# Performance work log

Measured on AMD Instinct MI355X. Metric: run time of the kernel, lower is better.

The kernel has to match this reference:

```python
import jax, jax.numpy as jnp
import numpy as np

N_NODES = 100000
N_EDGES = 3200000
IN_DIM = 128
OUT_DIM = 128


def setup_inputs() -> dict:
    key = jax.random.key(0)
    k1, k2, k3, k4, k5 = jax.random.split(key, 5)
    fea_input = jax.random.normal(k1, (N_NODES, IN_DIM), dtype=jnp.float32)
    edge_row = jax.random.randint(k2, (N_EDGES,), 0, N_NODES, dtype=jnp.int32)
    edge_col = jax.random.randint(k3, (N_EDGES,), 0, N_NODES, dtype=jnp.int32)
    edge_val = jax.random.uniform(k4, (N_EDGES,), dtype=jnp.float32)
    # kaiming_uniform-style init for weight, zeros for bias
    bound = float(np.sqrt(6.0 / IN_DIM))
    weight = jax.random.uniform(k5, (IN_DIM, OUT_DIM), dtype=jnp.float32,
                                minval=-bound, maxval=bound)
    bias = jnp.zeros((OUT_DIM,), dtype=jnp.float32)
    return {
        "fea_input": fea_input,
        "edge_row": edge_row,
        "edge_col": edge_col,
        "edge_val": edge_val,
        "weight": weight,
        "bias": bias,
    }


def reference(fea_input, edge_row, edge_col, edge_val, weight, bias):
    # support = X @ W  -> [N, OUT_DIM]
    support = jnp.matmul(fea_input, weight)
    # SpMM: out[r] += val * support[c] for each edge (r, c, val)
    gathered = support[edge_col] * edge_val[:, None]  # [E, OUT_DIM]
    output = jax.ops.segment_sum(gathered, edge_row, num_segments=N_NODES)
    return output + bias
```

## Files before the change

kernel.cpp:

```cpp
#include <hip/hip_runtime.h>
#include <hip/hip_bf16.h>


#define N_NODES 100000
#define N_EDGES 3200000
#define DIM 128
#define RB 16
#define RPB 128
#define NBKT ((N_NODES + RPB - 1) / RPB)
#define CHUNK 8192
#define NCHK ((N_EDGES + CHUNK - 1) / CHUNK)
#define CAP2 5376

typedef __attribute__((ext_vector_type(8))) short bf16x8;
typedef __attribute__((ext_vector_type(4))) float f32x4;
typedef unsigned long long u64;
typedef unsigned int u32;

__device__ inline ushort bf16rne(float f) {
  uint32_t u = __float_as_uint(f);
  u += 0x7fffu + ((u >> 16) & 1u);
  return (ushort)(u >> 16);
}
__device__ inline float lofl(u32 u) { return __uint_as_float(u << 16); }
__device__ inline float hifl(u32 u) { return __uint_as_float(u & 0xffff0000u); }

__global__ __launch_bounds__(256) void prep_count_kernel(
    const float* __restrict__ X, const float* __restrict__ W,
    ushort* __restrict__ Xh, ushort* __restrict__ Wh,
    const int* __restrict__ erow, int* __restrict__ bcnt,
    int* __restrict__ table) {
  __shared__ int cnt[NBKT];
  if (blockIdx.x < 1024) {
    const size_t nx4 = (size_t)N_NODES * DIM / 4;
    const size_t nw4 = (size_t)DIM * DIM / 4;
    for (size_t i = (size_t)blockIdx.x * blockDim.x + threadIdx.x;
         i < nx4 + nw4; i += (size_t)1024 * blockDim.x) {
      const float4 f = (i < nx4) ? ((const float4*)X)[i] : ((const float4*)W)[i - nx4];
      ushort4 h;
      h.x = bf16rne(f.x); h.y = bf16rne(f.y); h.z = bf16rne(f.z); h.w = bf16rne(f.w);
      if (i < nx4) ((ushort4*)Xh)[i] = h;
      else         ((ushort4*)Wh)[i - nx4] = h;
    }
  } else {
    const int cb = blockIdx.x - 1024;
    for (int b = threadIdx.x; b < NBKT; b += 256) cnt[b] = 0;
    __syncthreads();
    const int e0 = cb * CHUNK;
    #pragma unroll
    for (int it = 0; it < CHUNK / 256; ++it) {
      const int e = e0 + it * 256 + threadIdx.x;
      if (e < N_EDGES) atomicAdd(&cnt[erow[e] >> 7], 1);
    }
    __syncthreads();
    for (int b = threadIdx.x; b < NBKT; b += 256) {
      const int c = cnt[b];
      table[(size_t)cb * NBKT + b] = c;
      if (c) atomicAdd(&bcnt[b], c);
    }
  }
}

__global__ __launch_bounds__(1024) void bscan_kernel(int* __restrict__ bcur,
                                                     int* __restrict__ bbase) {
  __shared__ int wsum[16];
  const int t = threadIdx.x, lane = t & 63, wid = t >> 6;
  const int v = (t < NBKT) ? bcur[t] : 0;
  int incl = v;
  #pragma unroll
  for (int off = 1; off < 64; off <<= 1) {
    int n = __shfl_up(incl, off, 64);
    if (lane >= off) incl += n;
  }
  if (lane == 63) wsum[wid] = incl;
  __syncthreads();
  if (t == 0) {
    int s = 0;
    #pragma unroll
    for (int w = 0; w < 16; ++w) { int x = wsum[w]; wsum[w] = s; s += x; }
  }
  __syncthreads();
  const int excl = wsum[wid] + incl - v;
  if (t < NBKT) { bbase[t] = excl; bcur[t] = excl; }
  if (t == NBKT - 1) bbase[NBKT] = excl + v;
}

__global__ __launch_bounds__(256) void partition_kernel(
    const int* __restrict__ erow, const int* __restrict__ ecol,
    const float* __restrict__ eval, const int* __restrict__ table,
    int* __restrict__ bcur, u64* __restrict__ p64) {
  __shared__ int cnt[NBKT];
  const int e0 = blockIdx.x * CHUNK;
  for (int b = threadIdx.x; b < NBKT; b += 256) {
    const int c = table[(size_t)blockIdx.x * NBKT + b];
    cnt[b] = c ? atomicAdd(&bcur[b], c) : 0;
  }
  __syncthreads();
  #pragma unroll
  for (int it = 0; it < CHUNK / 256; ++it) {
    const int e = e0 + it * 256 + threadIdx.x;
    if (e < N_EDGES) {
      const int r = erow[e];
      const u32 lo = ((u32)ecol[e] << 15) | (u32)bf16rne(eval[e]);
      const int p = atomicAdd(&cnt[r >> 7], 1);
      p64[p] = ((u64)(r & (RPB - 1)) << 32) | (u64)lo;
    }
  }
}

__global__ __launch_bounds__(512) void agg_sort_kernel(
    const ushort* __restrict__ Xh,
    const int* __restrict__ bbase, const u64* __restrict__ p64,
    ushort* __restrict__ Yh) {
  __shared__ u32 sbuf[CAP2 + 16];
  __shared__ int hist[RPB];
  __shared__ int rstart[RPB];
  __shared__ int curs[RPB];
  __shared__ int wtot;
  const int b = blockIdx.x, t = threadIdx.x;
  const int s = bbase[b];
  int nE = bbase[b + 1] - s;
  if (nE > CAP2) nE = CAP2;

  if (t < RPB) hist[t] = 0;
  __syncthreads();
  for (int i = t; i < nE; i += 512)
    atomicAdd(&hist[(int)(p64[s + i] >> 32) & (RPB - 1)], 1);
  __syncthreads();
  int v = 0, incl = 0;
  if (t < RPB) {
    v = hist[t];
    incl = v;
    #pragma unroll
    for (int off = 1; off < 64; off <<= 1) {
      int n = __shfl_up(incl, off, 64);
      if ((t & 63) >= off) incl += n;
    }
    if (t == 63) wtot = incl;
  }
  __syncthreads();
  if (t < RPB) {
    const int e = incl - v + ((t >= 64) ? wtot : 0);
    rstart[t] = e;
    curs[t] = e;
  }
  __syncthreads();
  for (int i = t; i < nE; i += 512) {
    const u64 w = p64[s + i];
    const int p = atomicAdd(&curs[(int)(w >> 32) & (RPB - 1)], 1);
    sbuf[p] = (u32)w;
  }
  __syncthreads();

  const int wid = t >> 6, lane = t & 63;
  const int q = lane >> 4;
  const u32 sub16 = (u32)(lane & 15) * 16u;
  const char* Xb = (const char*)Xh;
  #pragma unroll 1
  for (int j = 0; j < 16; ++j) {
    const int rl = wid * 16 + j;
    const int gr = b * RPB + rl;
    if (gr >= N_NODES) break;
    const int s0 = rstart[rl];
    const int s1 = s0 + hist[rl];
    float f0 = 0.f, f1 = 0.f, f2 = 0.f, f3 = 0.f;
    float f4 = 0.f, f5 = 0.f, f6 = 0.f, f7 = 0.f;
    #pragma unroll 1
    for (int e = s0 + q; e < s1; e += 16) {
      const u32 lo0 = sbuf[e];
      const u32 lo1 = (e + 4  < s1) ? sbuf[e + 4]  : 0u;
      const u32 lo2 = (e + 8  < s1) ? sbuf[e + 8]  : 0u;
      const u32 lo3 = (e + 12 < s1) ? sbuf[e + 12] : 0u;
      const u32 o0 = (lo0 >> 7) & 0xFFFFFF00u;
      const u32 o1 = (lo1 >> 7) & 0xFFFFFF00u;
      const u32 o2 = (lo2 >> 7) & 0xFFFFFF00u;
      const u32 o3 = (lo3 >> 7) & 0xFFFFFF00u;
      const uint4 g0 = *(const uint4*)(Xb + (o0 + sub16));
      const uint4 g1 = *(const uint4*)(Xb + (o1 + sub16));
      const uint4 g2 = *(const uint4*)(Xb + (o2 + sub16));
      const uint4 g3 = *(const uint4*)(Xb + (o3 + sub16));
      const float v0 = __uint_as_float((lo0 & 0x7fffu) << 16);
      const float v1 = __uint_as_float((lo1 & 0x7fffu) << 16);
      const float v2 = __uint_as_float((lo2 & 0x7fffu) << 16);
      const float v3 = __uint_as_float((lo3 & 0x7fffu) << 16);
      f0 += v0 * lofl(g0.x); f1 += v0 * hifl(g0.x);
      f2 += v0 * lofl(g0.y); f3 += v0 * hifl(g0.y);
      f4 += v0 * lofl(g0.z); f5 += v0 * hifl(g0.z);
      f6 += v0 * lofl(g0.w); f7 += v0 * hifl(g0.w);
      f0 += v1 * lofl(g1.x); f1 += v1 * hifl(g1.x);
      f2 += v1 * lofl(g1.y); f3 += v1 * hifl(g1.y);
      f4 += v1 * lofl(g1.z); f5 += v1 * hifl(g1.z);
      f6 += v1 * lofl(g1.w); f7 += v1 * hifl(g1.w);
      f0 += v2 * lofl(g2.x); f1 += v2 * hifl(g2.x);
      f2 += v2 * lofl(g2.y); f3 += v2 * hifl(g2.y);
      f4 += v2 * lofl(g2.z); f5 += v2 * hifl(g2.z);
      f6 += v2 * lofl(g2.w); f7 += v2 * hifl(g2.w);
      f0 += v3 * lofl(g3.x); f1 += v3 * hifl(g3.x);
      f2 += v3 * lofl(g3.y); f3 += v3 * hifl(g3.y);
      f4 += v3 * lofl(g3.z); f5 += v3 * hifl(g3.z);
      f6 += v3 * lofl(g3.w); f7 += v3 * hifl(g3.w);
    }
    f0 += __shfl_xor(f0, 16); f1 += __shfl_xor(f1, 16);
    f2 += __shfl_xor(f2, 16); f3 += __shfl_xor(f3, 16);
    f4 += __shfl_xor(f4, 16); f5 += __shfl_xor(f5, 16);
    f6 += __shfl_xor(f6, 16); f7 += __shfl_xor(f7, 16);
    f0 += __shfl_xor(f0, 32); f1 += __shfl_xor(f1, 32);
    f2 += __shfl_xor(f2, 32); f3 += __shfl_xor(f3, 32);
    f4 += __shfl_xor(f4, 32); f5 += __shfl_xor(f5, 32);
    f6 += __shfl_xor(f6, 32); f7 += __shfl_xor(f7, 32);
    if (lane < 16) {
      uint4 o;
      o.x = (u32)bf16rne(f0) | ((u32)bf16rne(f1) << 16);
      o.y = (u32)bf16rne(f2) | ((u32)bf16rne(f3) << 16);
      o.z = (u32)bf16rne(f4) | ((u32)bf16rne(f5) << 16);
      o.w = (u32)bf16rne(f6) | ((u32)bf16rne(f7) << 16);
      ((uint4*)(Yh + (size_t)gr * DIM))[lane] = o;
    }
  }
}

__global__ __launch_bounds__(256) void gemm_mfma(const ushort* __restrict__ Yh,
                                                 const ushort* __restrict__ Wh,
                                                 const float* __restrict__ bias,
                                                 float* __restrict__ out) {
  const int wid = threadIdx.x >> 6, lane = threadIdx.x & 63;
  const int lr = lane & 15, lq = lane >> 4;
  const int n0 = wid * 32;

  bf16x8 bfrag[4][2];
  float bval[2];
  #pragma unroll
  for (int nt = 0; nt < 2; ++nt) {
    const int col = n0 + nt * 16 + lr;
    bval[nt] = bias[col];
    #pragma unroll
    for (int kk = 0; kk < 4; ++kk) {
      const int kbase = kk * 32 + lq * 8;
      bf16x8 b;
      #pragma unroll
      for (int i = 0; i < 8; ++i)
        b[i] = (short)Wh[(size_t)(kbase + i) * DIM + col];
      bfrag[kk][nt] = b;
    }
  }

  const int r0 = blockIdx.x * 256;
  #pragma unroll 1
  for (int g = 0; g < 16; ++g) {
    const int m0 = r0 + g * 16;
    if (m0 >= N_NODES) break;
    bf16x8 afrag[4];
    const ushort* arow = Yh + (size_t)(m0 + lr) * DIM + lq * 8;
    #pragma unroll
    for (int kk = 0; kk < 4; ++kk)
      afrag[kk] = *(const bf16x8*)(arow + kk * 32);
    #pragma unroll
    for (int nt = 0; nt < 2; ++nt) {
      f32x4 acc = {0.f, 0.f, 0.f, 0.f};
      #pragma unroll
      for (int kk = 0; kk < 4; ++kk)
        acc = __builtin_amdgcn_mfma_f32_16x16x32_bf16(afrag[kk], bfrag[kk][nt], acc, 0, 0, 0);
      const int col = n0 + nt * 16 + lr;
      #pragma unroll
      for (int j = 0; j < 4; ++j)
        out[(size_t)(m0 + lq * 4 + j) * DIM + col] = acc[j] + bval[nt];
    }
  }
}

__global__ __launch_bounds__(128) void gemm_kernel(
    const float* __restrict__ IN, const float* __restrict__ W,
    float* __restrict__ OUT, const float* __restrict__ bias, int add_bias) {
  __shared__ float Wsh[DIM * DIM];
  __shared__ float Xsh[RB * DIM];
  const int t = threadIdx.x;
  #pragma unroll 8
  for (int i = 0; i < DIM; ++i) Wsh[i * DIM + t] = W[i * DIM + t];
  const int r0 = blockIdx.x * RB;
  #pragma unroll
  for (int idx = t; idx < RB * DIM; idx += 128)
    Xsh[idx] = IN[(size_t)r0 * DIM + idx];
  __syncthreads();
  float acc[RB];
  const float b = add_bias ? bias[t] : 0.f;
  #pragma unroll
  for (int r = 0; r < RB; ++r) acc[r] = b;
  for (int k = 0; k < DIM; ++k) {
    const float w = Wsh[k * DIM + t];
    #pragma unroll
    for (int r = 0; r < RB; ++r) acc[r] += Xsh[r * DIM + k] * w;
  }
  #pragma unroll
  for (int r = 0; r < RB; ++r)
    OUT[(size_t)(r0 + r) * DIM + t] = acc[r];
}

__global__ void init_kernel(float* __restrict__ out, const float* __restrict__ bias) {
  const size_t total4 = (size_t)N_NODES * DIM / 4;
  const float4* b4 = (const float4*)bias;
  float4* o4 = (float4*)out;
  for (size_t i = (size_t)blockIdx.x * blockDim.x + threadIdx.x;
       i < total4; i += (size_t)gridDim.x * blockDim.x)
    o4[i] = b4[i & 31];
}

__global__ __launch_bounds__(256) void scatter_kernel(
    const float* __restrict__ S,
    const int* __restrict__ erow, const int* __restrict__ ecol,
    const float* __restrict__ eval, float* __restrict__ out) {
  const long long g = (long long)blockIdx.x * blockDim.x + threadIdx.x;
  const long long e = g >> 5;
  const int lane = (int)(g & 31);
  if (e >= N_EDGES) return;
  const int r = erow[e];
  const int c = ecol[e];
  const float v = eval[e];
  const float4 x = ((const float4*)(S + (size_t)c * DIM))[lane];
  float* o = out + (size_t)r * DIM + lane * 4;
  atomicAdd(o + 0, v * x.x);
  atomicAdd(o + 1, v * x.y);
  atomicAdd(o + 2, v * x.z);
  atomicAdd(o + 3, v * x.w);
}

extern "C" void kernel_launch(void* const* d_in, const int* in_sizes, int n_in,
                              void* d_out, int out_size, void* d_ws, size_t ws_size,
                              hipStream_t stream) {
  const float* X    = (const float*)d_in[0];
  const int*   erow = (const int*)d_in[1];
  const int*   ecol = (const int*)d_in[2];
  const float* eval = (const float*)d_in[3];
  const float* W    = (const float*)d_in[4];
  const float* bias = (const float*)d_in[5];
  float* out = (float*)d_out;

  const size_t P64_BYTES = (size_t)N_EDGES * 8;
  const size_t XH_BYTES  = (size_t)N_NODES * DIM * 2;
  const size_t YH_BYTES  = (size_t)N_NODES * DIM * 2;
  const size_t WH_BYTES  = (size_t)DIM * DIM * 2;
  const size_t BB_BYTES  = (size_t)(NBKT + 1) * 4;
  const size_t BC_BYTES  = (size_t)NBKT * 4;
  const size_t NEED = P64_BYTES + XH_BYTES + YH_BYTES + WH_BYTES +
                      BB_BYTES + BC_BYTES + 256;

  if (ws_size >= NEED) {
    char* w = (char*)d_ws;
    u64*    p64     = (u64*)w;     w += P64_BYTES;
    ushort* Xh      = (ushort*)w;  w += XH_BYTES;
    ushort* Yh      = (ushort*)w;  w += YH_BYTES;
    ushort* Wh      = (ushort*)w;  w += WH_BYTES;
    int*    bbase   = (int*)w;     w += BB_BYTES;
    int*    bcur    = (int*)w;
    int*    table   = (int*)Yh;

    hipMemsetAsync(bcur, 0, BC_BYTES, stream);
    prep_count_kernel<<<1024 + NCHK, 256, 0, stream>>>(X, W, Xh, Wh, erow, bcur, table);
    bscan_kernel<<<1, 1024, 0, stream>>>(bcur, bbase);
    partition_kernel<<<NCHK, 256, 0, stream>>>(erow, ecol, eval, table, bcur, p64);
    agg_sort_kernel<<<NBKT, 512, 0, stream>>>(Xh, bbase, p64, Yh);
    gemm_mfma<<<(N_NODES + 255) / 256, 256, 0, stream>>>(Yh, Wh, bias, out);
  } else {
    float* S = (float*)d_ws;
    init_kernel<<<2048, 256, 0, stream>>>(out, bias);
    gemm_kernel<<<N_NODES / RB, 128, 0, stream>>>(X, W, S, bias, 0);
    const long long threads = (long long)N_EDGES * 32;
    scatter_kernel<<<(int)((threads + 255) / 256), 256, 0, stream>>>(S, erow, ecol, eval, out);
  }
}
```

Measured before the change: 233.4 us.

## Halve row bucket size and sort edges by column group for gather locality

Buckets now hold 64 destination rows instead of 128, and the bucket scan handles two elements per thread to cover the larger bucket count. Inside the aggregation kernel, edges are sorted by a compound key of local row and the top bits of the column index. Each warp then sweeps the column groups in order for its 8 rows, accumulating in a register array, so gathers of source features from Xh are clustered by column range and cache reuse should improve. The cost is more registers (64 accumulators per thread), a larger shared histogram and scan, and an unrolled inner loop that may lower occupancy or per-edge ILP.

```diff
diff --git a/kernel.cpp b/kernel.cpp
--- a/kernel.cpp
+++ b/kernel.cpp
@@ -6,11 +6,12 @@
 #define N_EDGES 3200000
 #define DIM 128
 #define RB 16
-#define RPB 128
+#define RPB 64
 #define NBKT ((N_NODES + RPB - 1) / RPB)
 #define CHUNK 8192
 #define NCHK ((N_EDGES + CHUNK - 1) / CHUNK)
-#define CAP2 5376
+#define NGRP 16
+#define CAP3 2688
 
 typedef __attribute__((ext_vector_type(8))) short bf16x8;
 typedef __attribute__((ext_vector_type(4))) float f32x4;
@@ -50,7 +51,7 @@
     #pragma unroll
     for (int it = 0; it < CHUNK / 256; ++it) {
       const int e = e0 + it * 256 + threadIdx.x;
-      if (e < N_EDGES) atomicAdd(&cnt[erow[e] >> 7], 1);
+      if (e < N_EDGES) atomicAdd(&cnt[erow[e] >> 6], 1);
     }
     __syncthreads();
     for (int b = threadIdx.x; b < NBKT; b += 256) {
@@ -63,26 +64,30 @@
 
 __global__ __launch_bounds__(1024) void bscan_kernel(int* __restrict__ bcur,
                                                      int* __restrict__ bbase) {
-  __shared__ int wsum[16];
+  __shared__ int wsum[32];
   const int t = threadIdx.x, lane = t & 63, wid = t >> 6;
-  const int v = (t < NBKT) ? bcur[t] : 0;
-  int incl = v;
+  int v0 = (t < NBKT) ? bcur[t] : 0;
+  int v1 = (t + 1024 < NBKT) ? bcur[t + 1024] : 0;
+  int i0 = v0, i1 = v1;
   #pragma unroll
   for (int off = 1; off < 64; off <<= 1) {
-    int n = __shfl_up(incl, off, 64);
-    if (lane >= off) incl += n;
-  }
-  if (lane == 63) wsum[wid] = incl;
+    int n0 = __shfl_up(i0, off, 64);
+    int n1 = __shfl_up(i1, off, 64);
+    if (lane >= off) { i0 += n0; i1 += n1; }
+  }
+  if (lane == 63) { wsum[wid] = i0; wsum[16 + wid] = i1; }
   __syncthreads();
   if (t == 0) {
     int s = 0;
     #pragma unroll
-    for (int w = 0; w < 16; ++w) { int x = wsum[w]; wsum[w] = s; s += x; }
-  }
-  __syncthreads();
-  const int excl = wsum[wid] + incl - v;
-  if (t < NBKT) { bbase[t] = excl; bcur[t] = excl; }
-  if (t == NBKT - 1) bbase[NBKT] = excl + v;
+    for (int k = 0; k < 32; ++k) { int x = wsum[k]; wsum[k] = s; s += x; }
+    bbase[NBKT] = s;
+  }
+  __syncthreads();
+  const int e0 = wsum[wid] + i0 - v0;
+  const int e1 = wsum[16 + wid] + i1 - v1;
+  if (t < NBKT) { bbase[t] = e0; bcur[t] = e0; }
+  if (t + 1024 < NBKT) { bbase[t + 1024] = e1; bcur[t + 1024] = e1; }
 }
 
 __global__ __launch_bounds__(256) void partition_kernel(
@@ -102,7 +107,7 @@
     if (e < N_EDGES) {
       const int r = erow[e];
       const u32 lo = ((u32)ecol[e] << 15) | (u32)bf16rne(eval[e]);
-      const int p = atomicAdd(&cnt[r >> 7], 1);
+      const int p = atomicAdd(&cnt[r >> 6], 1);
       p64[p] = ((u64)(r & (RPB - 1)) << 32) | (u64)lo;
     }
   }
@@ -112,108 +117,96 @@
     const ushort* __restrict__ Xh,
     const int* __restrict__ bbase, const u64* __restrict__ p64,
     ushort* __restrict__ Yh) {
-  __shared__ u32 sbuf[CAP2 + 16];
-  __shared__ int hist[RPB];
-  __shared__ int rstart[RPB];
-  __shared__ int curs[RPB];
-  __shared__ int wtot;
+  __shared__ u32 sbuf[CAP3];
+  __shared__ int hist[RPB * NGRP];
+  __shared__ int rstart[RPB * NGRP];
+  __shared__ int curs[RPB * NGRP];
+  __shared__ int wsum[16];
   const int b = blockIdx.x, t = threadIdx.x;
+  const int lane = t & 63, wid = t >> 6;
   const int s = bbase[b];
   int nE = bbase[b + 1] - s;
-  if (nE > CAP2) nE = CAP2;
-
-  if (t < RPB) hist[t] = 0;
-  __syncthreads();
-  for (int i = t; i < nE; i += 512)
-    atomicAdd(&hist[(int)(p64[s + i] >> 32) & (RPB - 1)], 1);
-  __syncthreads();
-  int v = 0, incl = 0;
-  if (t < RPB) {
-    v = hist[t];
-    incl = v;
-    #pragma unroll
-    for (int off = 1; off < 64; off <<= 1) {
-      int n = __shfl_up(incl, off, 64);
-      if ((t & 63) >= off) incl += n;
-    }
-    if (t == 63) wtot = incl;
-  }
-  __syncthreads();
-  if (t < RPB) {
-    const int e = incl - v + ((t >= 64) ? wtot : 0);
-    rstart[t] = e;
-    curs[t] = e;
-  }
+  if (nE > CAP3) nE = CAP3;
+
+  hist[t] = 0; hist[t + 512] = 0;
   __syncthreads();
   for (int i = t; i < nE; i += 512) {
     const u64 w = p64[s + i];
-    const int p = atomicAdd(&curs[(int)(w >> 32) & (RPB - 1)], 1);
-    sbuf[p] = (u32)w;
-  }
-  __syncthreads();
-
-  const int wid = t >> 6, lane = t & 63;
+    const int key = (((int)(w >> 32) & 63) << 4) | (int)((u32)w >> 28);
+    atomicAdd(&hist[key], 1);
+  }
+  __syncthreads();
+  int v0 = hist[t], v1 = hist[t + 512];
+  int i0 = v0, i1 = v1;
+  #pragma unroll
+  for (int off = 1; off < 64; off <<= 1) {
+    int n0 = __shfl_up(i0, off, 64);
+    int n1 = __shfl_up(i1, off, 64);
+    if (lane >= off) { i0 += n0; i1 += n1; }
+  }
+  if (lane == 63) { wsum[wid] = i0; wsum[8 + wid] = i1; }
+  __syncthreads();
+  if (t == 0) {
+    int sa = 0;
+    #pragma unroll
+    for (int k = 0; k < 16; ++k) { int x = wsum[k]; wsum[k] = sa; sa += x; }
+  }
+  __syncthreads();
+  const int ex0 = wsum[wid] + i0 - v0;
+  const int ex1 = wsum[8 + wid] + i1 - v1;
+  rstart[t] = ex0; curs[t] = ex0;
+  rstart[t + 512] = ex1; curs[t + 512] = ex1;
+  __syncthreads();
+  for (int i = t; i < nE; i += 512) {
+    const u64 w = p64[s + i];
+    const int key = (((int)(w >> 32) & 63) << 4) | (int)((u32)w >> 28);
+    sbuf[atomicAdd(&curs[key], 1)] = (u32)w;
+  }
+  __syncthreads();
+
   const int q = lane >> 4;
   const u32 sub16 = (u32)(lane & 15) * 16u;
   const char* Xb = (const char*)Xh;
+  const int rbase = wid * 8;
+  float f[8][8];
+  #pragma unroll
+  for (int j = 0; j < 8; ++j)
+    #pragma unroll
+    for (int k = 0; k < 8; ++k) f[j][k] = 0.f;
+
   #pragma unroll 1
-  for (int j = 0; j < 16; ++j) {
-    const int rl = wid * 16 + j;
-    const int gr = b * RPB + rl;
-    if (gr >= N_NODES) break;
-    const int s0 = rstart[rl];
-    const int s1 = s0 + hist[rl];
-    float f0 = 0.f, f1 = 0.f, f2 = 0.f, f3 = 0.f;
-    float f4 = 0.f, f5 = 0.f, f6 = 0.f, f7 = 0.f;
-    #pragma unroll 1
-    for (int e = s0 + q; e < s1; e += 16) {
-      const u32 lo0 = sbuf[e];
-      const u32 lo1 = (e + 4  < s1) ? sbuf[e + 4]  : 0u;
-      const u32 lo2 = (e + 8  < s1) ? sbuf[e + 8]  : 0u;
-      const u32 lo3 = (e + 12 < s1) ? sbuf[e + 12] : 0u;
-      const u32 o0 = (lo0 >> 7) & 0xFFFFFF00u;
-      const u32 o1 = (lo1 >> 7) & 0xFFFFFF00u;
-      const u32 o2 = (lo2 >> 7) & 0xFFFFFF00u;
-      const u32 o3 = (lo3 >> 7) & 0xFFFFFF00u;
-      const uint4 g0 = *(const uint4*)(Xb + (o0 + sub16));
-      const uint4 g1 = *(const uint4*)(Xb + (o1 + sub16));
-      const uint4 g2 = *(const uint4*)(Xb + (o2 + sub16));
-      const uint4 g3 = *(const uint4*)(Xb + (o3 + sub16));
-      const float v0 = __uint_as_float((lo0 & 0x7fffu) << 16);
-      const float v1 = __uint_as_float((lo1 & 0x7fffu) << 16);
-      const float v2 = __uint_as_float((lo2 & 0x7fffu) << 16);
-      const float v3 = __uint_as_float((lo3 & 0x7fffu) << 16);
-      f0 += v0 * lofl(g0.x); f1 += v0 * hifl(g0.x);
-      f2 += v0 * lofl(g0.y); f3 += v0 * hifl(g0.y);
-      f4 += v0 * lofl(g0.z); f5 += v0 * hifl(g0.z);
-      f6 += v0 * lofl(g0.w); f7 += v0 * hifl(g0.w);
-      f0 += v1 * lofl(g1.x); f1 += v1 * hifl(g1.x);
-      f2 += v1 * lofl(g1.y); f3 += v1 * hifl(g1.y);
-      f4 += v1 * lofl(g1.z); f5 += v1 * hifl(g1.z);
-      f6 += v1 * lofl(g1.w); f7 += v1 * hifl(g1.w);
-      f0 += v2 * lofl(g2.x); f1 += v2 * hifl(g2.x);
-      f2 += v2 * lofl(g2.y); f3 += v2 * hifl(g2.y);
-      f4 += v2 * lofl(g2.z); f5 += v2 * hifl(g2.z);
-      f6 += v2 * lofl(g2.w); f7 += v2 * hifl(g2.w);
-      f0 += v3 * lofl(g3.x); f1 += v3 * hifl(g3.x);
-      f2 += v3 * lofl(g3.y); f3 += v3 * hifl(g3.y);
-      f4 += v3 * lofl(g3.z); f5 += v3 * hifl(g3.z);
-      f6 += v3 * lofl(g3.w); f7 += v3 * hifl(g3.w);
-    }
-    f0 += __shfl_xor(f0, 16); f1 += __shfl_xor(f1, 16);
-    f2 += __shfl_xor(f2, 16); f3 += __shfl_xor(f3, 16);
-    f4 += __shfl_xor(f4, 16); f5 += __shfl_xor(f5, 16);
-    f6 += __shfl_xor(f6, 16); f7 += __shfl_xor(f7, 16);
-    f0 += __shfl_xor(f0, 32); f1 += __shfl_xor(f1, 32);
-    f2 += __shfl_xor(f2, 32); f3 += __shfl_xor(f3, 32);
-    f4 += __shfl_xor(f4, 32); f5 += __shfl_xor(f5, 32);
-    f6 += __shfl_xor(f6, 32); f7 += __shfl_xor(f7, 32);
-    if (lane < 16) {
+  for (int g = 0; g < 13; ++g) {
+    #pragma unroll
+    for (int j = 0; j < 8; ++j) {
+      const int key = ((rbase + j) << 4) | g;
+      const int s0 = rstart[key];
+      const int s1 = s0 + hist[key];
+      for (int e = s0 + q; e < s1; e += 4) {
+        const u32 lo = sbuf[e];
+        const uint4 gq = *(const uint4*)(Xb + (((lo >> 7) & 0xFFFFFF00u) + sub16));
+        const float v = __uint_as_float((lo & 0x7fffu) << 16);
+        f[j][0] += v * lofl(gq.x); f[j][1] += v * hifl(gq.x);
+        f[j][2] += v * lofl(gq.y); f[j][3] += v * hifl(gq.y);
+        f[j][4] += v * lofl(gq.z); f[j][5] += v * hifl(gq.z);
+        f[j][6] += v * lofl(gq.w); f[j][7] += v * hifl(gq.w);
+      }
+    }
+  }
+
+  #pragma unroll
+  for (int j = 0; j < 8; ++j) {
+    #pragma unroll
+    for (int k = 0; k < 8; ++k) {
+      f[j][k] += __shfl_xor(f[j][k], 16);
+      f[j][k] += __shfl_xor(f[j][k], 32);
+    }
+    const int gr = b * RPB + rbase + j;
+    if (gr < N_NODES && lane < 16) {
       uint4 o;
-      o.x = (u32)bf16rne(f0) | ((u32)bf16rne(f1) << 16);
-      o.y = (u32)bf16rne(f2) | ((u32)bf16rne(f3) << 16);
-      o.z = (u32)bf16rne(f4) | ((u32)bf16rne(f5) << 16);
-      o.w = (u32)bf16rne(f6) | ((u32)bf16rne(f7) << 16);
+      o.x = (u32)bf16rne(f[j][0]) | ((u32)bf16rne(f[j][1]) << 16);
+      o.y = (u32)bf16rne(f[j][2]) | ((u32)bf16rne(f[j][3]) << 16);
+      o.z = (u32)bf16rne(f[j][4]) | ((u32)bf16rne(f[j][5]) << 16);
+      o.w = (u32)bf16rne(f[j][6]) | ((u32)bf16rne(f[j][7]) << 16);
       ((uint4*)(Yh + (size_t)gr * DIM))[lane] = o;
     }
   }
```

Measured after the change: 325.0 us. 1.39x slower.
